# Kernel tuning notes

Measured on AMD Instinct MI355X. Metric: run time of the kernel, lower is better.

The kernel has to match this reference:

```python
import jax, jax.numpy as jnp
import numpy as np

B, N, F_DIM, OUT_DIM = 8, 2048, 128, 128

def setup_inputs() -> dict:
    key = jax.random.key(0)
    k1, k2, k3, k4, k5 = jax.random.split(key, 5)
    return {
        "x": jax.random.normal(k1, (B, N, F_DIM), dtype=jnp.float32),
        "adj_w": jax.random.normal(k2, (2 * F_DIM,), dtype=jnp.float32) * (1.0 / np.sqrt(2 * F_DIM)),
        "adj_b": jax.random.normal(k3, (), dtype=jnp.float32),
        "weight": jax.random.normal(k4, (F_DIM, OUT_DIM), dtype=jnp.float32) * (1.0 / np.sqrt(F_DIM)),
        "bias": jax.random.normal(k5, (OUT_DIM,), dtype=jnp.float32),
    }

def reference(x, adj_w, adj_b, weight, bias):
    # x: [B, N, F]. adj[b,i,j] = Linear(concat(x_i, x_j)) = x_i@w1 + x_j@w2 + b
    Bb, Nn, Ff = x.shape
    a_i = x @ adj_w[:Ff]           # [B, N]
    a_j = x @ adj_w[Ff:]           # [B, N]
    adj = a_i[:, :, None] + a_j[:, None, :] + adj_b   # [B, N, N]
    adj = adj + jnp.eye(Nn, dtype=adj.dtype)          # adj[:, i, i] += 1
    out = x @ weight                                  # [B, N, out]
    deg_inv_sqrt = jnp.maximum(adj.sum(axis=-1), 1.0) ** -0.5  # clamp(min=1).pow(-0.5)
    adj = deg_inv_sqrt[:, :, None] * adj * deg_inv_sqrt[:, None, :]
    out = jnp.matmul(adj, out) + bias
    return jax.nn.relu(out)
```

## Files before the change

kernel.cpp:

```cpp
#include <hip/hip_runtime.h>

#define N_ 2048
#define F_ 128

#define WS_P1 0
#define WS_P2 512

typedef __attribute__((ext_vector_type(8))) short short8v;
typedef __attribute__((ext_vector_type(4))) float f32x4;
typedef unsigned long long u64;

__device__ inline short f2bf(float f) {
    union { float f; unsigned u; } c; c.f = f;
    unsigned r = (c.u + 0x7FFFu + ((c.u >> 16) & 1u)) >> 16;
    return (short)r;
}
__device__ inline float bf2f(short h) {
    union { unsigned u; float f; } c;
    c.u = ((unsigned)(unsigned short)h) << 16;
    return c.f;
}
__device__ inline void store_pair(u64* p, float f) {
    union { float f; unsigned u; } c; c.f = f;
    const u64 v = ((u64)(~c.u) << 32) | (u64)c.u;
    __hip_atomic_store(p, v, __ATOMIC_RELAXED, __HIP_MEMORY_SCOPE_AGENT);
}
__device__ inline bool pair_ok(u64 v) {
    return (unsigned)(v >> 32) == (unsigned)(~(unsigned)v);
}
__device__ inline float pair_val(u64 v) {
    union { unsigned u; float f; } c; c.u = (unsigned)v;
    return c.f;
}

__global__ __launch_bounds__(256, 2) void gcn_one(
    const float* __restrict__ x, const float* __restrict__ adj_w,
    const float* __restrict__ adj_b_p, const float* __restrict__ weight,
    const float* __restrict__ bias, float* __restrict__ outx,
    u64* __restrict__ P1, u64* __restrict__ P2)
{
    __shared__ unsigned short wt[128 * 128];
    __shared__ float adjw[256];
    __shared__ float ail[32], ajl[32];
    __shared__ float disl[32], ajdl[32];
    __shared__ float red0[2][128], red1[2][128];
    __shared__ float t0l[128], t1l[128], s0l[128], s1l[128], bl[128];
    __shared__ float Ash;

    const int bid = blockIdx.x;
    const int b = bid >> 6, kbme = bid & 63, r0 = kbme * 32;
    const int t = threadIdx.x;
    const int lane = t & 63, w = t >> 6;
    const int u = lane & 15, g = lane >> 4;

    adjw[t] = adj_w[t];
    if (t < 128) bl[t] = bias[t];
    __syncthreads();

    {
        const int row = t >> 3, kseg = t & 7;
        const float* xp = x + (size_t)(b * N_ + r0 + row) * F_ + kseg * 16;
        float ai = 0.f, aj = 0.f;
        #pragma unroll
        for (int p = 0; p < 4; ++p) {
            const float4 v = *reinterpret_cast<const float4*>(xp + p * 4);
            const float vv[4] = {v.x, v.y, v.z, v.w};
            #pragma unroll
            for (int q = 0; q < 4; ++q) {
                const int k = kseg * 16 + p * 4 + q;
                ai = fmaf(vv[q], adjw[k], ai);
                aj = fmaf(vv[q], adjw[128 + k], aj);
            }
        }
        #pragma unroll
        for (int m = 1; m < 8; m <<= 1) {
            ai += __shfl_xor(ai, m, 64);
            aj += __shfl_xor(aj, m, 64);
        }
        if (kseg == 0) { ail[row] = ai + adj_b_p[0]; ajl[row] = aj; }
    }
    __syncthreads();
    if (t < 32) {
        float s = ajl[t];
        #pragma unroll
        for (int off = 16; off > 0; off >>= 1) s += __shfl_down(s, off, 64);
        if (t == 0) store_pair(&P1[bid], s);
    }

    {
        const int c = t & 127, khalf = t >> 7;
        for (int j8 = 0; j8 < 8; ++j8) {
            const int kb = khalf * 8 + j8;
            short8v v;
            #pragma unroll
            for (int i = 0; i < 8; ++i)
                v[i] = f2bf(weight[(kb * 8 + i) * F_ + c]);
            const int slot = kb ^ (c & 15);
            *reinterpret_cast<short8v*>(&wt[c * 128 + slot * 8]) = v;
        }
    }
    __syncthreads();

    const int wr = (w & 1) * 16;
    const int ct0 = (w >> 1) * 4;
    f32x4 acc[4];
    #pragma unroll
    for (int i = 0; i < 4; ++i) acc[i] = (f32x4)(0.f);
    {
        const float* xrow = x + (size_t)(b * N_ + r0 + wr + u) * F_;
        #pragma unroll
        for (int kk = 0; kk < 4; ++kk) {
            const float4 xa = *reinterpret_cast<const float4*>(xrow + kk * 32 + g * 8);
            const float4 xb = *reinterpret_cast<const float4*>(xrow + kk * 32 + g * 8 + 4);
            short8v af;
            af[0] = f2bf(xa.x); af[1] = f2bf(xa.y); af[2] = f2bf(xa.z); af[3] = f2bf(xa.w);
            af[4] = f2bf(xb.x); af[5] = f2bf(xb.y); af[6] = f2bf(xb.z); af[7] = f2bf(xb.w);
            const int kb = kk * 4 + g;
            #pragma unroll
            for (int c = 0; c < 4; ++c) {
                const int col = (ct0 + c) * 16 + u;
                const int slot = kb ^ u;
                const short8v bfv = *reinterpret_cast<const short8v*>(&wt[col * 128 + slot * 8]);
                acc[c] = __builtin_amdgcn_mfma_f32_16x16x32_bf16(af, bfv, acc[c], 0, 0, 0);
            }
        }
    }

    if (t < 64) {
        u64 v;
        do {
            v = __hip_atomic_load(&P1[b * 64 + t], __ATOMIC_RELAXED, __HIP_MEMORY_SCOPE_AGENT);
        } while (!pair_ok(v));
        float s = pair_val(v);
        #pragma unroll
        for (int off = 32; off > 0; off >>= 1) s += __shfl_down(s, off, 64);
        if (t == 0) Ash = s;
    }
    __syncthreads();
    if (t < 32) {
        const float deg = fmaxf(2048.f * ail[t] + Ash + 1.f, 1.f);
        const float d = rsqrtf(deg);
        disl[t] = d;
        ajdl[t] = ajl[t] * d;
    }
    __syncthreads();

    {
        const int c = t & 127, gh = t >> 7;
        float s0 = 0.f, s1 = 0.f;
        const float* xp = x + (size_t)(b * N_ + r0 + gh * 16) * F_;
        #pragma unroll 4
        for (int r = 0; r < 16; ++r) {
            const float v = xp[r * F_ + c];
            s0 = fmaf(disl[gh * 16 + r], v, s0);
            s1 = fmaf(ajdl[gh * 16 + r], v, s1);
        }
        red0[gh][c] = s0;
        red1[gh][c] = s1;
    }
    __syncthreads();
    if (t < 128) {
        const size_t rec = ((size_t)(b * 64 + kbme) * 128 + t) * 2;
        store_pair(&P2[rec], red0[0][t] + red0[1][t]);
        store_pair(&P2[rec + 1], red1[0][t] + red1[1][t]);
    }
    __syncthreads();

    {
        const int c = t & 127, kh = t >> 7;
        float s0 = 0.f, s1 = 0.f;
        #pragma unroll 1
        for (int kb0 = 0; kb0 < 32; kb0 += 8) {
            u64 v0[8], v1[8];
            bool ok;
            do {
                ok = true;
                #pragma unroll
                for (int i = 0; i < 8; ++i) {
                    const size_t rec = ((size_t)(b * 64 + kh * 32 + kb0 + i) * 128 + c) * 2;
                    v0[i] = __hip_atomic_load(&P2[rec], __ATOMIC_RELAXED, __HIP_MEMORY_SCOPE_AGENT);
                    v1[i] = __hip_atomic_load(&P2[rec + 1], __ATOMIC_RELAXED, __HIP_MEMORY_SCOPE_AGENT);
                }
                #pragma unroll
                for (int i = 0; i < 8; ++i) ok &= pair_ok(v0[i]) & pair_ok(v1[i]);
                if (!ok) __builtin_amdgcn_s_sleep(1);
            } while (!ok);
            #pragma unroll
            for (int i = 0; i < 8; ++i) { s0 += pair_val(v0[i]); s1 += pair_val(v1[i]); }
        }
        red0[kh][c] = s0;
        red1[kh][c] = s1;
    }
    __syncthreads();
    if (t < 128) t0l[t] = red0[0][t] + red0[1][t];
    else { const int c = t - 128; t1l[c] = red1[0][c] + red1[1][c]; }
    __syncthreads();

    {
        const int c = t & 127;
        const float* tv = (t < 128) ? t0l : t1l;
        float sacc = 0.f;
        for (int kb = 0; kb < 16; ++kb) {
            const int slot = kb ^ (c & 15);
            const short8v v = *reinterpret_cast<const short8v*>(&wt[c * 128 + slot * 8]);
            #pragma unroll
            for (int i = 0; i < 8; ++i)
                sacc = fmaf(tv[kb * 8 + i], bf2f(v[i]), sacc);
        }
        if (t < 128) s0l[c] = sacc; else s1l[c] = sacc;
    }
    __syncthreads();

    #pragma unroll
    for (int c = 0; c < 4; ++c) {
        const int col = (ct0 + c) * 16 + u;
        const float sv0 = s0l[col], sv1 = s1l[col], bv = bl[col];
        #pragma unroll
        for (int r = 0; r < 4; ++r) {
            const int row = wr + g * 4 + r;
            const float d = disl[row], ab = ail[row];
            const float o = fmaxf(d * (ab * sv0 + sv1 + d * acc[c][r]) + bv, 0.f);
            outx[(size_t)(b * N_ + r0 + row) * F_ + col] = o;
        }
    }
}

extern "C" void kernel_launch(void* const* d_in, const int* in_sizes, int n_in,
                              void* d_out, int out_size, void* d_ws, size_t ws_size,
                              hipStream_t stream) {
    const float* x      = (const float*)d_in[0];
    const float* adj_w  = (const float*)d_in[1];
    const float* adj_b  = (const float*)d_in[2];
    const float* weight = (const float*)d_in[3];
    const float* bias   = (const float*)d_in[4];
    float* out = (float*)d_out;
    u64* ws = (u64*)d_ws;

    gcn_one<<<512, 256, 0, stream>>>(x, adj_w, adj_b, weight, bias, out,
                                     ws + WS_P1, ws + WS_P2);
}
```

Measured before the change: 20.93 us.

## Reuse MFMA accumulators for column sums and add two-level cross-block reduction

The per-block partial sums (disl·xW and ajdl·xW) are now computed directly from the MFMA accumulator tile, so x is no longer re-read and the separate weight-multiply GEMV is gone. Instead of every block gathering all 64 partials for its batch, four designated blocks per batch reduce one slice of columns each and publish the final sums to a new SF buffer, which all blocks then poll. Spin loops get s_sleep backoff. This cuts redundant global polling traffic and compute, but the partials now come from the bf16-rounded product and a second dependency level is added to the grid-wide handoff.

```diff
diff --git a/kernel.cpp b/kernel.cpp
--- a/kernel.cpp
+++ b/kernel.cpp
@@ -4,7 +4,8 @@
 #define F_ 128
 
 #define WS_P1 0
-#define WS_P2 512
+#define WS_SF 512
+#define WS_P2 2560
 
 typedef __attribute__((ext_vector_type(8))) short short8v;
 typedef __attribute__((ext_vector_type(4))) float f32x4;
@@ -15,11 +16,6 @@
     unsigned r = (c.u + 0x7FFFu + ((c.u >> 16) & 1u)) >> 16;
     return (short)r;
 }
-__device__ inline float bf2f(short h) {
-    union { unsigned u; float f; } c;
-    c.u = ((unsigned)(unsigned short)h) << 16;
-    return c.f;
-}
 __device__ inline void store_pair(u64* p, float f) {
     union { float f; unsigned u; } c; c.f = f;
     const u64 v = ((u64)(~c.u) << 32) | (u64)c.u;
@@ -37,14 +33,14 @@
     const float* __restrict__ x, const float* __restrict__ adj_w,
     const float* __restrict__ adj_b_p, const float* __restrict__ weight,
     const float* __restrict__ bias, float* __restrict__ outx,
-    u64* __restrict__ P1, u64* __restrict__ P2)
+    u64* __restrict__ P1, u64* __restrict__ SF, u64* __restrict__ P2)
 {
     __shared__ unsigned short wt[128 * 128];
     __shared__ float adjw[256];
     __shared__ float ail[32], ajl[32];
     __shared__ float disl[32], ajdl[32];
-    __shared__ float red0[2][128], red1[2][128];
-    __shared__ float t0l[128], t1l[128], s0l[128], s1l[128], bl[128];
+    __shared__ float red0[4][64], red1[4][64];
+    __shared__ float s0l[128], s1l[128], bl[128];
     __shared__ float Ash;
 
     const int bid = blockIdx.x;
@@ -128,9 +124,11 @@
 
     if (t < 64) {
         u64 v;
-        do {
+        while (true) {
             v = __hip_atomic_load(&P1[b * 64 + t], __ATOMIC_RELAXED, __HIP_MEMORY_SCOPE_AGENT);
-        } while (!pair_ok(v));
+            if (pair_ok(v)) break;
+            __builtin_amdgcn_s_sleep(2);
+        }
         float s = pair_val(v);
         #pragma unroll
         for (int off = 32; off > 0; off >>= 1) s += __shfl_down(s, off, 64);
@@ -146,68 +144,71 @@
     __syncthreads();
 
     {
-        const int c = t & 127, gh = t >> 7;
-        float s0 = 0.f, s1 = 0.f;
-        const float* xp = x + (size_t)(b * N_ + r0 + gh * 16) * F_;
-        #pragma unroll 4
-        for (int r = 0; r < 16; ++r) {
-            const float v = xp[r * F_ + c];
-            s0 = fmaf(disl[gh * 16 + r], v, s0);
-            s1 = fmaf(ajdl[gh * 16 + r], v, s1);
-        }
-        red0[gh][c] = s0;
-        red1[gh][c] = s1;
-    }
-    __syncthreads();
-    if (t < 128) {
-        const size_t rec = ((size_t)(b * 64 + kbme) * 128 + t) * 2;
-        store_pair(&P2[rec], red0[0][t] + red0[1][t]);
-        store_pair(&P2[rec + 1], red1[0][t] + red1[1][t]);
-    }
-    __syncthreads();
-
-    {
-        const int c = t & 127, kh = t >> 7;
-        float s0 = 0.f, s1 = 0.f;
-        #pragma unroll 1
-        for (int kb0 = 0; kb0 < 32; kb0 += 8) {
-            u64 v0[8], v1[8];
-            bool ok;
-            do {
-                ok = true;
-                #pragma unroll
-                for (int i = 0; i < 8; ++i) {
-                    const size_t rec = ((size_t)(b * 64 + kh * 32 + kb0 + i) * 128 + c) * 2;
-                    v0[i] = __hip_atomic_load(&P2[rec], __ATOMIC_RELAXED, __HIP_MEMORY_SCOPE_AGENT);
-                    v1[i] = __hip_atomic_load(&P2[rec + 1], __ATOMIC_RELAXED, __HIP_MEMORY_SCOPE_AGENT);
-                }
-                #pragma unroll
-                for (int i = 0; i < 8; ++i) ok &= pair_ok(v0[i]) & pair_ok(v1[i]);
-                if (!ok) __builtin_amdgcn_s_sleep(1);
-            } while (!ok);
-            #pragma unroll
-            for (int i = 0; i < 8; ++i) { s0 += pair_val(v0[i]); s1 += pair_val(v1[i]); }
-        }
-        red0[kh][c] = s0;
-        red1[kh][c] = s1;
-    }
-    __syncthreads();
-    if (t < 128) t0l[t] = red0[0][t] + red0[1][t];
-    else { const int c = t - 128; t1l[c] = red1[0][c] + red1[1][c]; }
-    __syncthreads();
-
-    {
-        const int c = t & 127;
-        const float* tv = (t < 128) ? t0l : t1l;
-        float sacc = 0.f;
-        for (int kb = 0; kb < 16; ++kb) {
-            const int slot = kb ^ (c & 15);
-            const short8v v = *reinterpret_cast<const short8v*>(&wt[c * 128 + slot * 8]);
-            #pragma unroll
-            for (int i = 0; i < 8; ++i)
-                sacc = fmaf(tv[kb * 8 + i], bf2f(v[i]), sacc);
-        }
-        if (t < 128) s0l[c] = sacc; else s1l[c] = sacc;
+        float p0[4], p1[4];
+        #pragma unroll
+        for (int c = 0; c < 4; ++c) {
+            float s0 = 0.f, s1 = 0.f;
+            #pragma unroll
+            for (int r = 0; r < 4; ++r) {
+                const int row = wr + g * 4 + r;
+                s0 = fmaf(disl[row], acc[c][r], s0);
+                s1 = fmaf(ajdl[row], acc[c][r], s1);
+            }
+            s0 += __shfl_xor(s0, 16, 64); s0 += __shfl_xor(s0, 32, 64);
+            s1 += __shfl_xor(s1, 16, 64); s1 += __shfl_xor(s1, 32, 64);
+            p0[c] = s0; p1[c] = s1;
+        }
+        if (g == 0) {
+            #pragma unroll
+            for (int c = 0; c < 4; ++c) {
+                red0[w][c * 16 + u] = p0[c];
+                red1[w][c * 16 + u] = p1[c];
+            }
+        }
+    }
+    __syncthreads();
+    {
+        const int c = t & 127, vec = t >> 7;
+        const int cg = c >> 6, cc = c & 63;
+        const float v = (vec == 0)
+            ? (red0[2 * cg][cc] + red0[2 * cg + 1][cc])
+            : (red1[2 * cg][cc] + red1[2 * cg + 1][cc]);
+        store_pair(&P2[((size_t)((b * 128 + c) * 2 + vec) << 6) + kbme], v);
+    }
+
+    if (kbme < 4) {
+        const int p = t >> 2, klo = (t & 3) * 16;
+        const int c = kbme * 32 + (p >> 1), vec = p & 1;
+        u64* base = &P2[(size_t)((b * 128 + c) * 2 + vec) << 6];
+        u64 vv[16];
+        bool ok;
+        do {
+            ok = true;
+            #pragma unroll
+            for (int i = 0; i < 16; ++i)
+                vv[i] = __hip_atomic_load(&base[klo + i], __ATOMIC_RELAXED, __HIP_MEMORY_SCOPE_AGENT);
+            #pragma unroll
+            for (int i = 0; i < 16; ++i) ok &= pair_ok(vv[i]);
+            if (!ok) __builtin_amdgcn_s_sleep(4);
+        } while (!ok);
+        float s = 0.f;
+        #pragma unroll
+        for (int i = 0; i < 16; ++i) s += pair_val(vv[i]);
+        s += __shfl_xor(s, 1, 64);
+        s += __shfl_xor(s, 2, 64);
+        if ((t & 3) == 0)
+            store_pair(&SF[(b * 128 + c) * 2 + vec], s);
+    }
+
+    {
+        const int c = t & 127, vec = t >> 7;
+        u64 v;
+        while (true) {
+            v = __hip_atomic_load(&SF[(b * 128 + c) * 2 + vec], __ATOMIC_RELAXED, __HIP_MEMORY_SCOPE_AGENT);
+            if (pair_ok(v)) break;
+            __builtin_amdgcn_s_sleep(2);
+        }
+        if (vec == 0) s0l[c] = pair_val(v); else s1l[c] = pair_val(v);
     }
     __syncthreads();
 
@@ -237,5 +238,5 @@
     u64* ws = (u64*)d_ws;
 
     gcn_one<<<512, 256, 0, stream>>>(x, adj_w, adj_b, weight, bias, out,
-                                     ws + WS_P1, ws + WS_P2);
-}
+                                     ws + WS_P1, ws + WS_SF, ws + WS_P2);
+}
```

Measured after the change: 22.26 us. 6.4% more time.
